# Kernel optimization log

Measured on AMD Instinct MI355X. Metric: run time of the kernel, lower is better.

The kernel has to match this reference:

```python
import jax, jax.numpy as jnp
import numpy as np
from jax import lax

B, OBS, E, H = 65536, 20, 64, 64


def setup_inputs() -> dict:
    key = jax.random.key(0)
    ks = jax.random.split(key, 13)
    s = 0.1
    inp = {
        "obs_traj": jax.random.normal(ks[0], (B, OBS, 2), jnp.float32),
        "W_emb": jax.random.normal(ks[1], (E, 2), jnp.float32) * s,
        "b_emb": jax.random.normal(ks[2], (E,), jnp.float32) * s,
        "Wih_e": jax.random.normal(ks[3], (4 * H, E), jnp.float32) * s,
        "Whh_e": jax.random.normal(ks[4], (4 * H, H), jnp.float32) * s,
        "bih_e": jax.random.normal(ks[5], (4 * H,), jnp.float32) * s,
        "bhh_e": jax.random.normal(ks[6], (4 * H,), jnp.float32) * s,
        "Wih_d": jax.random.normal(ks[7], (4 * H, E), jnp.float32) * s,
        "Whh_d": jax.random.normal(ks[8], (4 * H, H), jnp.float32) * s,
        "bih_d": jax.random.normal(ks[9], (4 * H,), jnp.float32) * s,
        "bhh_d": jax.random.normal(ks[10], (4 * H,), jnp.float32) * s,
        "W_fc": jax.random.normal(ks[11], (2, H), jnp.float32) * s,
        "b_fc": jax.random.normal(ks[12], (2,), jnp.float32) * s,
        "pred_len": 12,
    }
    return inp


def _lstm_step(x, h, c, Wih, Whh, b):
    # PyTorch LSTM gate order: i, f, g, o
    g = x @ Wih.T + h @ Whh.T + b  # [B, 4H]
    i, f, gg, o = jnp.split(g, 4, axis=-1)
    c2 = jax.nn.sigmoid(f) * c + jax.nn.sigmoid(i) * jnp.tanh(gg)
    h2 = jax.nn.sigmoid(o) * jnp.tanh(c2)
    return h2, c2


def reference(obs_traj, W_emb, b_emb, Wih_e, Whh_e, bih_e, bhh_e,
              Wih_d, Whh_d, bih_d, bhh_d, W_fc, b_fc, pred_len):
    bsz = obs_traj.shape[0]
    dt = obs_traj.dtype
    # Encoder: embed all observed steps at once, then scan the LSTM over time.
    emb = jax.nn.relu(obs_traj @ W_emb.T + b_emb)  # [B, OBS, E]
    b_e = bih_e + bhh_e
    h0 = jnp.zeros((bsz, H), dt)
    c0 = jnp.zeros((bsz, H), dt)

    def enc_step(carry, x_t):
        h, c = carry
        h, c = _lstm_step(x_t, h, c, Wih_e, Whh_e, b_e)
        return (h, c), None

    (h, c), _ = lax.scan(enc_step, (h0, c0), jnp.swapaxes(emb, 0, 1))

    b_d = bih_d + bhh_d
    dec_in = jax.nn.relu(obs_traj[:, -1, :] @ W_emb.T + b_emb)  # [B, E]

    def dec_step(carry, _):
        h, c, x = carry
        h, c = _lstm_step(x, h, c, Wih_d, Whh_d, b_d)
        pred = h @ W_fc.T + b_fc  # [B, 2]
        nxt = jax.nn.relu(pred @ W_emb.T + b_emb)
        return (h, c, nxt), pred

    _, preds = lax.scan(dec_step, (h, c, dec_in), None, length=pred_len)
    return jnp.swapaxes(preds, 0, 1)  # [B, pred_len, 2]
```

## Files before the change

### kernel.cpp

```cpp
#include <hip/hip_runtime.h>

typedef __bf16 bf16x8 __attribute__((ext_vector_type(8)));
typedef __bf16 bf16x4 __attribute__((ext_vector_type(4)));
typedef float  f32x4  __attribute__((ext_vector_type(4)));
typedef float  f32x2  __attribute__((ext_vector_type(2)));

constexpr int OBS   = 20;
constexpr int PRED  = 12;
constexpr int AST   = 136;
constexpr int GRID  = 1024;

constexpr float SIO = -1.4426950408889634f;
constexpr float SG  =  2.8853900817779268f;

__device__ __forceinline__ float exp2_(float x) { return __builtin_amdgcn_exp2f(x); }
__device__ __forceinline__ float rcp_(float x)  { return __builtin_amdgcn_rcpf(x); }

struct SmallW {
    float  biasf_e[256];
    float  biasf_d[256];
    float4 embc[64];
    float  wfc[128];
    float  bfc[2];
};

__device__ __forceinline__ void load_bfr(bf16x8 (&bfr)[4][3],
                                         const float* Wih, const float* Whh,
                                         int wblk, int m, int q) {
    #pragma unroll
    for (int c = 0; c < 4; ++c) {
        const float sc = (c == 2) ? SG : SIO;
        const int n = c * 64 + wblk + m;
        #pragma unroll
        for (int kt = 0; kt < 3; ++kt) {
            const float* s = (kt < 2) ? (Wih + n * 64 + kt * 32 + q * 8)
                                      : (Whh + n * 64 + q * 8);
            float4 a = *(const float4*)s;
            float4 b = *(const float4*)(s + 4);
            bf16x8 v;
            v[0] = (__bf16)(sc * a.x); v[1] = (__bf16)(sc * a.y);
            v[2] = (__bf16)(sc * a.z); v[3] = (__bf16)(sc * a.w);
            v[4] = (__bf16)(sc * b.x); v[5] = (__bf16)(sc * b.y);
            v[6] = (__bf16)(sc * b.z); v[7] = (__bf16)(sc * b.w);
            bfr[c][kt] = v;
        }
    }
}

__device__ __forceinline__ void fill_wkt3(bf16x8* wkt3, const float* Whh,
                                          int wv, int lane, int wblk, int m, int q) {
    #pragma unroll
    for (int c = 0; c < 4; ++c) {
        const float sc = (c == 2) ? SG : SIO;
        const int n = c * 64 + wblk + m;
        const float* s = Whh + n * 64 + 32 + q * 8;
        float4 a = *(const float4*)s;
        float4 b = *(const float4*)(s + 4);
        bf16x8 v;
        v[0] = (__bf16)(sc * a.x); v[1] = (__bf16)(sc * a.y);
        v[2] = (__bf16)(sc * a.z); v[3] = (__bf16)(sc * a.w);
        v[4] = (__bf16)(sc * b.x); v[5] = (__bf16)(sc * b.y);
        v[6] = (__bf16)(sc * b.z); v[7] = (__bf16)(sc * b.w);
        wkt3[(wv * 4 + c) * 64 + lane] = v;
    }
}

template<int NSUB>
__device__ void lstm_body(__bf16* As, bf16x8* wkt3, float* pred_s, SmallW& sw,
                          const float* obs,
                          const float* Wih_e, const float* Whh_e,
                          const float* Wih_d, const float* Whh_d,
                          float* out, size_t gRow0)
{
    constexpr int CH = NSUB * 16;
    constexpr int NP = (NSUB + 1) / 2;
    const int tid  = threadIdx.x;
    const int wv   = tid >> 6;
    const int lane = tid & 63;
    const int m    = lane & 15;
    const int q    = lane >> 4;
    const int wblk = wv * 16;

    bf16x8 bfr[4][3];
    load_bfr(bfr, Wih_e, Whh_e, wblk, m, q);

    f32x4 cst[2 * NSUB];
    #pragma unroll
    for (int i = 0; i < 2 * NSUB; ++i) cst[i] = f32x4{0.f, 0.f, 0.f, 0.f};

    f32x4 acc[NSUB][4];

    auto gemm = [&](int chunk, const float* bfrag) {
        #pragma unroll
        for (int c = 0; c < 4; ++c) {
            f32x4 b = *(const f32x4*)&bfrag[(wv * 4 + c) * 16 + q * 4];
            #pragma unroll
            for (int s = 0; s < NSUB; ++s) acc[s][c] = b;
        }
        #pragma unroll
        for (int kt = 0; kt < 3; ++kt) {
            bf16x8 af[NSUB];
            #pragma unroll
            for (int s = 0; s < NSUB; ++s)
                af[s] = *(const bf16x8*)&As[(chunk * CH + s * 16 + m) * AST + kt * 32 + q * 8];
            #pragma unroll
            for (int s = 0; s < NSUB; ++s)
                #pragma unroll
                for (int c = 0; c < 4; ++c)
                    acc[s][c] = __builtin_amdgcn_mfma_f32_16x16x32_bf16(bfr[c][kt], af[s], acc[s][c], 0, 0, 0);
        }
        {
            bf16x8 af[NSUB];
            #pragma unroll
            for (int s = 0; s < NSUB; ++s)
                af[s] = *(const bf16x8*)&As[(chunk * CH + s * 16 + m) * AST + 96 + q * 8];
            #pragma unroll
            for (int c = 0; c < 4; ++c) {
                bf16x8 w3 = wkt3[(wv * 4 + c) * 64 + lane];
                #pragma unroll
                for (int s = 0; s < NSUB; ++s)
                    acc[s][c] = __builtin_amdgcn_mfma_f32_16x16x32_bf16(w3, af[s], acc[s][c], 0, 0, 0);
            }
        }
    };

    auto update = [&](int chunk) {
        #pragma unroll
        for (int sub = 0; sub < NSUB; ++sub) {
            const int idx = chunk * NSUB + sub;
            const int row = chunk * CH + sub * 16 + m;
            f32x4 ci = cst[idx];
            bf16x4 h4;
            #pragma unroll
            for (int r = 0; r < 4; ++r) {
                const float gi = acc[sub][0][r];
                const float gf = acc[sub][1][r];
                const float gg = acc[sub][2][r];
                const float go = acc[sub][3][r];
                const float Ef = exp2_(gf);
                const float a  = ci[r] * rcp_(1.0f + Ef);
                const float Ei = exp2_(gi);
                const float Eg = exp2_(gg);
                const float d1 = 1.0f + Ei;
                const float r1 = rcp_(fmaf(d1, Eg, d1));
                const float cN = fmaf(Eg - 1.0f, r1, a);
                const float Eo = exp2_(go);
                const float Ec = exp2_(cN * SG);
                const float d2 = 1.0f + Eo;
                const float r2 = rcp_(fmaf(d2, Ec, d2));
                const float h  = (Ec - 1.0f) * r2;
                ci[r] = cN;
                h4[r] = (__bf16)h;
            }
            cst[idx] = ci;
            *(bf16x4*)&As[row * AST + 64 + wblk + q * 4] = h4;
        }
    };

    auto emb_enc = [&](int chunk, int t) {
        const int h8 = lane >> 5;
        #pragma unroll
        for (int p = 0; p < NP; ++p) {
            const int rloc = p * 32 + (lane & 31);
            if (rloc < CH) {
                const int row = chunk * CH + rloc;
                f32x2 ov = *(const f32x2*)(obs + (gRow0 + row) * (OBS * 2) + t * 2);
                bf16x8 v;
                #pragma unroll
                for (int j = 0; j < 8; ++j) {
                    float4 wc = sw.embc[wblk + h8 * 8 + j];
                    v[j] = (__bf16)fmaxf(fmaf(ov[0], wc.x, fmaf(ov[1], wc.y, wc.z)), 0.f);
                }
                *(bf16x8*)&As[row * AST + wblk + h8 * 8] = v;
            }
        }
    };

    __syncthreads();

    emb_enc(0, 0);
    emb_enc(1, 0);
    __syncthreads();
    gemm(0, sw.biasf_e);

    for (int t = 0; t < OBS; ++t) {
        __syncthreads();
        update(0);
        gemm(1, sw.biasf_e);
        if (t + 1 < OBS) emb_enc(0, t + 1);
        __syncthreads();
        update(1);
        if (t + 1 < OBS) {
            gemm(0, sw.biasf_e);
            emb_enc(1, t + 1);
        }
    }

    load_bfr(bfr, Wih_d, Whh_d, wblk, m, q);
    fill_wkt3(wkt3, Whh_d, wv, lane, wblk, m, q);
    gemm(0, sw.biasf_d);

    auto pred_phase = [&](int chunk, int td) {
        const int comp = (tid >> 2) & 1;
        const int seg  = tid & 3;
        #pragma unroll
        for (int p = 0; p < NP; ++p) {
            const int rloc = p * 32 + (tid >> 3);
            const int row  = chunk * CH + rloc;
            const bool act = (rloc < CH);
            float pv = 0.f;
            if (act) {
                bf16x8 h0 = *(const bf16x8*)&As[row * AST + 64 + seg * 16];
                bf16x8 h1 = *(const bf16x8*)&As[row * AST + 64 + seg * 16 + 8];
                f32x4 w0 = *(const f32x4*)&sw.wfc[comp * 64 + seg * 16];
                f32x4 w1 = *(const f32x4*)&sw.wfc[comp * 64 + seg * 16 + 4];
                f32x4 w2 = *(const f32x4*)&sw.wfc[comp * 64 + seg * 16 + 8];
                f32x4 w3 = *(const f32x4*)&sw.wfc[comp * 64 + seg * 16 + 12];
                pv = (float)h0[0] * w0[0] + (float)h0[1] * w0[1] + (float)h0[2] * w0[2] + (float)h0[3] * w0[3]
                   + (float)h0[4] * w1[0] + (float)h0[5] * w1[1] + (float)h0[6] * w1[2] + (float)h0[7] * w1[3]
                   + (float)h1[0] * w2[0] + (float)h1[1] * w2[1] + (float)h1[2] * w2[2] + (float)h1[3] * w2[3]
                   + (float)h1[4] * w3[0] + (float)h1[5] * w3[1] + (float)h1[6] * w3[2] + (float)h1[7] * w3[3];
            }
            pv += __shfl_xor(pv, 1, 64);
            pv += __shfl_xor(pv, 2, 64);
            if (act && seg == 0) {
                pv += sw.bfc[comp];
                pred_s[row * 2 + comp] = pv;
                out[((gRow0 + row) * PRED + td) * 2 + comp] = pv;
            }
        }
    };
    auto emb_dec = [&](int chunk) {
        const int h8 = lane >> 5;
        #pragma unroll
        for (int p = 0; p < NP; ++p) {
            const int rloc = p * 32 + (lane & 31);
            if (rloc < CH) {
                const int row = chunk * CH + rloc;
                f32x2 pv = *(const f32x2*)&pred_s[row * 2];
                bf16x8 v;
                #pragma unroll
                for (int j = 0; j < 8; ++j) {
                    float4 wc = sw.embc[wblk + h8 * 8 + j];
                    v[j] = (__bf16)fmaxf(fmaf(pv[0], wc.x, fmaf(pv[1], wc.y, wc.z)), 0.f);
                }
                *(bf16x8*)&As[row * AST + wblk + h8 * 8] = v;
            }
        }
    };

    for (int td = 0; td < PRED; ++td) {
        __syncthreads();
        update(0);
        gemm(1, sw.biasf_d);
        __syncthreads();
        update(1);
        pred_phase(0, td);
        __syncthreads();
        pred_phase(1, td);
        if (td + 1 < PRED) emb_dec(0);
        __syncthreads();
        if (td + 1 < PRED) {
            emb_dec(1);
            gemm(0, sw.biasf_d);
        }
    }
}

__global__ __launch_bounds__(256, 4)
void vanilla_lstm(const float* __restrict__ obs,
                  const float* __restrict__ W_emb, const float* __restrict__ b_emb,
                  const float* __restrict__ Wih_e, const float* __restrict__ Whh_e,
                  const float* __restrict__ bih_e, const float* __restrict__ bhh_e,
                  const float* __restrict__ Wih_d, const float* __restrict__ Whh_d,
                  const float* __restrict__ bih_d, const float* __restrict__ bhh_d,
                  const float* __restrict__ W_fc,  const float* __restrict__ b_fc,
                  float* __restrict__ out)
{
    __shared__ __align__(16) __bf16 As[64 * AST];
    __shared__ bf16x8 wkt3[1024];
    __shared__ __align__(16) float  pred_s[64 * 2];
    __shared__ SmallW sw;

    const int tid = threadIdx.x;

    {
        const int wv_ = tid >> 6, c_ = (tid >> 4) & 3, qr = tid & 15;
        const int g = c_ * 64 + wv_ * 16 + qr;
        const float sc = (c_ == 2) ? SG : SIO;
        sw.biasf_e[tid] = sc * (bih_e[g] + bhh_e[g]);
        sw.biasf_d[tid] = sc * (bih_d[g] + bhh_d[g]);
    }
    if (tid < 64)  sw.embc[tid] = make_float4(W_emb[2 * tid], W_emb[2 * tid + 1], b_emb[tid], 0.f);
    if (tid < 128) sw.wfc[tid]  = W_fc[tid];
    if (tid < 2)   sw.bfc[tid]  = b_fc[tid];

    {
        uint4 z; z.x = z.y = z.z = z.w = 0u;
        #pragma unroll
        for (int i = 0; i < 2; ++i) {
            const int idx = tid + i * 256;
            const int r = idx >> 3, o = idx & 7;
            *((uint4*)&As[r * AST + 64] + o) = z;
        }
    }

    {
        const int wv = tid >> 6, lane = tid & 63, m = lane & 15, q = lane >> 4;
        fill_wkt3(wkt3, Whh_e, wv, lane, wv * 16, m, q);
    }

    const int bid = blockIdx.x;
    lstm_body<2>(As, wkt3, pred_s, sw, obs, Wih_e, Whh_e, Wih_d, Whh_d,
                 out, (size_t)bid * 64);
}

extern "C" void kernel_launch(void* const* d_in, const int* in_sizes, int n_in,
                              void* d_out, int out_size, void* d_ws, size_t ws_size,
                              hipStream_t stream) {
    (void)in_sizes; (void)n_in; (void)d_ws; (void)ws_size; (void)out_size;
    const float* obs   = (const float*)d_in[0];
    const float* W_emb = (const float*)d_in[1];
    const float* b_emb = (const float*)d_in[2];
    const float* Wih_e = (const float*)d_in[3];
    const float* Whh_e = (const float*)d_in[4];
    const float* bih_e = (const float*)d_in[5];
    const float* bhh_e = (const float*)d_in[6];
    const float* Wih_d = (const float*)d_in[7];
    const float* Whh_d = (const float*)d_in[8];
    const float* bih_d = (const float*)d_in[9];
    const float* bhh_d = (const float*)d_in[10];
    const float* W_fc  = (const float*)d_in[11];
    const float* b_fc  = (const float*)d_in[12];
    float* o = (float*)d_out;

    dim3 grid(GRID), block(256);
    hipLaunchKernelGGL(vanilla_lstm, grid, block, 0, stream,
                       obs, W_emb, b_emb, Wih_e, Whh_e, bih_e, bhh_e,
                       Wih_d, Whh_d, bih_d, bhh_d, W_fc, b_fc, o);
}
```

Baseline: 297.9 us.

## Keep all weight fragments in registers, swizzle LDS rows, prefetch obs loads

New measurement: 359.1 us. 1.21x slower.

```diff
diff --git a/kernel.cpp b/kernel.cpp
--- a/kernel.cpp
+++ b/kernel.cpp
@@ -15,6 +15,10 @@
 
 __device__ __forceinline__ float exp2_(float x) { return __builtin_amdgcn_exp2f(x); }
 __device__ __forceinline__ float rcp_(float x)  { return __builtin_amdgcn_rcpf(x); }
+
+__device__ __forceinline__ int As_idx(int row, int col) {
+    return row * AST + (col ^ ((row & 3) << 3));
+}
 
 struct SmallW {
     float  biasf_e[256];
@@ -24,7 +28,7 @@
     float  bfc[2];
 };
 
-__device__ __forceinline__ void load_bfr(bf16x8 (&bfr)[4][3],
+__device__ __forceinline__ void load_bfr(bf16x8 (&bfr)[4][4],
                                          const float* Wih, const float* Whh,
                                          int wblk, int m, int q) {
     #pragma unroll
@@ -32,9 +36,9 @@
         const float sc = (c == 2) ? SG : SIO;
         const int n = c * 64 + wblk + m;
         #pragma unroll
-        for (int kt = 0; kt < 3; ++kt) {
+        for (int kt = 0; kt < 4; ++kt) {
             const float* s = (kt < 2) ? (Wih + n * 64 + kt * 32 + q * 8)
-                                      : (Whh + n * 64 + q * 8);
+                                      : (Whh + n * 64 + (kt - 2) * 32 + q * 8);
             float4 a = *(const float4*)s;
             float4 b = *(const float4*)(s + 4);
             bf16x8 v;
@@ -47,26 +51,8 @@
     }
 }
 
-__device__ __forceinline__ void fill_wkt3(bf16x8* wkt3, const float* Whh,
-                                          int wv, int lane, int wblk, int m, int q) {
-    #pragma unroll
-    for (int c = 0; c < 4; ++c) {
-        const float sc = (c == 2) ? SG : SIO;
-        const int n = c * 64 + wblk + m;
-        const float* s = Whh + n * 64 + 32 + q * 8;
-        float4 a = *(const float4*)s;
-        float4 b = *(const float4*)(s + 4);
-        bf16x8 v;
-        v[0] = (__bf16)(sc * a.x); v[1] = (__bf16)(sc * a.y);
-        v[2] = (__bf16)(sc * a.z); v[3] = (__bf16)(sc * a.w);
-        v[4] = (__bf16)(sc * b.x); v[5] = (__bf16)(sc * b.y);
-        v[6] = (__bf16)(sc * b.z); v[7] = (__bf16)(sc * b.w);
-        wkt3[(wv * 4 + c) * 64 + lane] = v;
-    }
-}
-
 template<int NSUB>
-__device__ void lstm_body(__bf16* As, bf16x8* wkt3, float* pred_s, SmallW& sw,
+__device__ void lstm_body(__bf16* As, float* pred_s, SmallW& sw,
                           const float* obs,
                           const float* Wih_e, const float* Whh_e,
                           const float* Wih_d, const float* Whh_d,
@@ -81,7 +67,7 @@
     const int q    = lane >> 4;
     const int wblk = wv * 16;
 
-    bf16x8 bfr[4][3];
+    bf16x8 bfr[4][4];
     load_bfr(bfr, Wih_e, Whh_e, wblk, m, q);
 
     f32x4 cst[2 * NSUB];
@@ -98,29 +84,16 @@
             for (int s = 0; s < NSUB; ++s) acc[s][c] = b;
         }
         #pragma unroll
-        for (int kt = 0; kt < 3; ++kt) {
+        for (int kt = 0; kt < 4; ++kt) {
             bf16x8 af[NSUB];
             #pragma unroll
             for (int s = 0; s < NSUB; ++s)
-                af[s] = *(const bf16x8*)&As[(chunk * CH + s * 16 + m) * AST + kt * 32 + q * 8];
+                af[s] = *(const bf16x8*)&As[As_idx(chunk * CH + s * 16 + m, kt * 32 + q * 8)];
             #pragma unroll
             for (int s = 0; s < NSUB; ++s)
                 #pragma unroll
                 for (int c = 0; c < 4; ++c)
                     acc[s][c] = __builtin_amdgcn_mfma_f32_16x16x32_bf16(bfr[c][kt], af[s], acc[s][c], 0, 0, 0);
-        }
-        {
-            bf16x8 af[NSUB];
-            #pragma unroll
-            for (int s = 0; s < NSUB; ++s)
-                af[s] = *(const bf16x8*)&As[(chunk * CH + s * 16 + m) * AST + 96 + q * 8];
-            #pragma unroll
-            for (int c = 0; c < 4; ++c) {
-                bf16x8 w3 = wkt3[(wv * 4 + c) * 64 + lane];
-                #pragma unroll
-                for (int s = 0; s < NSUB; ++s)
-                    acc[s][c] = __builtin_amdgcn_mfma_f32_16x16x32_bf16(w3, af[s], acc[s][c], 0, 0, 0);
-            }
         }
     };
 
@@ -153,51 +126,64 @@
                 h4[r] = (__bf16)h;
             }
             cst[idx] = ci;
-            *(bf16x4*)&As[row * AST + 64 + wblk + q * 4] = h4;
-        }
-    };
-
-    auto emb_enc = [&](int chunk, int t) {
+            *(bf16x4*)&As[As_idx(row, 64 + wblk + q * 4)] = h4;
+        }
+    };
+
+    auto load_obs = [&](int chunk, int t, f32x2* ov) {
+        #pragma unroll
+        for (int p = 0; p < NP; ++p) {
+            const int rloc = p * 32 + (lane & 31);
+            if (rloc < CH)
+                ov[p] = *(const f32x2*)(obs + (gRow0 + chunk * CH + rloc) * (OBS * 2) + t * 2);
+        }
+    };
+    auto emb_store = [&](int chunk, const f32x2* ov) {
         const int h8 = lane >> 5;
         #pragma unroll
         for (int p = 0; p < NP; ++p) {
             const int rloc = p * 32 + (lane & 31);
             if (rloc < CH) {
                 const int row = chunk * CH + rloc;
-                f32x2 ov = *(const f32x2*)(obs + (gRow0 + row) * (OBS * 2) + t * 2);
                 bf16x8 v;
                 #pragma unroll
                 for (int j = 0; j < 8; ++j) {
                     float4 wc = sw.embc[wblk + h8 * 8 + j];
-                    v[j] = (__bf16)fmaxf(fmaf(ov[0], wc.x, fmaf(ov[1], wc.y, wc.z)), 0.f);
+                    v[j] = (__bf16)fmaxf(fmaf(ov[p][0], wc.x, fmaf(ov[p][1], wc.y, wc.z)), 0.f);
                 }
-                *(bf16x8*)&As[row * AST + wblk + h8 * 8] = v;
+                *(bf16x8*)&As[As_idx(row, wblk + h8 * 8)] = v;
             }
         }
     };
 
     __syncthreads();
 
-    emb_enc(0, 0);
-    emb_enc(1, 0);
+    {
+        f32x2 o0[NP], o1[NP];
+        load_obs(0, 0, o0); load_obs(1, 0, o1);
+        emb_store(0, o0);   emb_store(1, o1);
+    }
     __syncthreads();
     gemm(0, sw.biasf_e);
 
     for (int t = 0; t < OBS; ++t) {
         __syncthreads();
+        f32x2 ovA[NP];
+        if (t + 1 < OBS) load_obs(0, t + 1, ovA);
         update(0);
         gemm(1, sw.biasf_e);
-        if (t + 1 < OBS) emb_enc(0, t + 1);
-        __syncthreads();
+        if (t + 1 < OBS) emb_store(0, ovA);
+        __syncthreads();
+        f32x2 ovB[NP];
+        if (t + 1 < OBS) load_obs(1, t + 1, ovB);
         update(1);
         if (t + 1 < OBS) {
             gemm(0, sw.biasf_e);
-            emb_enc(1, t + 1);
+            emb_store(1, ovB);
         }
     }
 
     load_bfr(bfr, Wih_d, Whh_d, wblk, m, q);
-    fill_wkt3(wkt3, Whh_d, wv, lane, wblk, m, q);
     gemm(0, sw.biasf_d);
 
     auto pred_phase = [&](int chunk, int td) {
@@ -210,8 +196,8 @@
             const bool act = (rloc < CH);
             float pv = 0.f;
             if (act) {
-                bf16x8 h0 = *(const bf16x8*)&As[row * AST + 64 + seg * 16];
-                bf16x8 h1 = *(const bf16x8*)&As[row * AST + 64 + seg * 16 + 8];
+                bf16x8 h0 = *(const bf16x8*)&As[As_idx(row, 64 + seg * 16)];
+                bf16x8 h1 = *(const bf16x8*)&As[As_idx(row, 64 + seg * 16 + 8)];
                 f32x4 w0 = *(const f32x4*)&sw.wfc[comp * 64 + seg * 16];
                 f32x4 w1 = *(const f32x4*)&sw.wfc[comp * 64 + seg * 16 + 4];
                 f32x4 w2 = *(const f32x4*)&sw.wfc[comp * 64 + seg * 16 + 8];
@@ -244,7 +230,7 @@
                     float4 wc = sw.embc[wblk + h8 * 8 + j];
                     v[j] = (__bf16)fmaxf(fmaf(pv[0], wc.x, fmaf(pv[1], wc.y, wc.z)), 0.f);
                 }
-                *(bf16x8*)&As[row * AST + wblk + h8 * 8] = v;
+                *(bf16x8*)&As[As_idx(row, wblk + h8 * 8)] = v;
             }
         }
     };
@@ -278,7 +264,6 @@
                   float* __restrict__ out)
 {
     __shared__ __align__(16) __bf16 As[64 * AST];
-    __shared__ bf16x8 wkt3[1024];
     __shared__ __align__(16) float  pred_s[64 * 2];
     __shared__ SmallW sw;
 
@@ -301,17 +286,12 @@
         for (int i = 0; i < 2; ++i) {
             const int idx = tid + i * 256;
             const int r = idx >> 3, o = idx & 7;
-            *((uint4*)&As[r * AST + 64] + o) = z;
-        }
-    }
-
-    {
-        const int wv = tid >> 6, lane = tid & 63, m = lane & 15, q = lane >> 4;
-        fill_wkt3(wkt3, Whh_e, wv, lane, wv * 16, m, q);
+            *(uint4*)&As[As_idx(r, 64 + o * 8)] = z;
+        }
     }
 
     const int bid = blockIdx.x;
-    lstm_body<2>(As, wkt3, pred_s, sw, obs, Wih_e, Whh_e, Wih_d, Whh_d,
+    lstm_body<2>(As, pred_s, sw, obs, Wih_e, Whh_e, Wih_d, Whh_d,
                  out, (size_t)bid * 64);
 }
 
```
